# Optimization experiments

Measured on AMD Instinct MI355X. Metric: run time of the kernel, lower is better.

## Reference

```python
import jax, jax.numpy as jnp
import numpy as np

TAU = 2.0
VTH = 1.0
EPS = 1e-5
T_STEPS = 64

@jax.custom_vjp
def spike_atan(x):
    # Heaviside spike with ATan surrogate gradient (spikingjelly surrogate.ATan, alpha=2.0)
    return (x >= 0.0).astype(x.dtype)

def _spike_fwd(x):
    return spike_atan(x), x

def _spike_bwd(x, g):
    # d/dx [1/pi * atan(pi/2 * alpha * x) + 1/2] with alpha=2 -> 1 / (1 + (pi*x)^2)
    return (g / (1.0 + (jnp.pi * x) ** 2),)

spike_atan.defvjp(_spike_fwd, _spike_bwd)

def bn_eval(x, g, b, m, v):
    return (x - m) * (g / jnp.sqrt(v + EPS)) + b

def setup_inputs() -> dict:
    key = jax.random.key(0)
    ks = jax.random.split(key, 16)
    N, C, L, H, NC = 16384, 22, 63, 64, 4
    D = C * L
    s1 = 1.0 / np.sqrt(D)
    s2 = 1.0 / np.sqrt(H)
    return {
        'x': jax.random.normal(ks[0], (N, C, L), jnp.float32),
        'fc1_w': jax.random.normal(ks[1], (H, D), jnp.float32) * s1,
        'fc1_b': jax.random.normal(ks[2], (H,), jnp.float32) * s1,
        'bn1_g': jax.random.uniform(ks[3], (H,), jnp.float32, 0.5, 1.5),
        'bn1_b': jax.random.normal(ks[4], (H,), jnp.float32) * 0.1,
        'bn1_m': jax.random.normal(ks[5], (H,), jnp.float32) * 0.1,
        'bn1_v': jax.random.uniform(ks[6], (H,), jnp.float32, 0.5, 1.5),
        'fc2_w': jax.random.normal(ks[7], (H, H), jnp.float32) * s2,
        'fc2_b': jax.random.normal(ks[8], (H,), jnp.float32) * s2,
        'bn2_g': jax.random.uniform(ks[9], (H,), jnp.float32, 0.5, 1.5),
        'bn2_b': jax.random.normal(ks[10], (H,), jnp.float32) * 0.1,
        'bn2_m': jax.random.normal(ks[11], (H,), jnp.float32) * 0.1,
        'bn2_v': jax.random.uniform(ks[12], (H,), jnp.float32, 0.5, 1.5),
        'cls_w': jax.random.normal(ks[13], (NC, H), jnp.float32) * s2,
        'cls_b': jax.random.normal(ks[14], (NC,), jnp.float32) * s2,
    }

def reference(x, fc1_w, fc1_b, bn1_g, bn1_b, bn1_m, bn1_v,
              fc2_w, fc2_b, bn2_g, bn2_b, bn2_m, bn2_v, cls_w, cls_b):
    N = x.shape[0]
    x_flat = x.reshape(N, -1)                       # [N, 1386]
    # fc1+bn1 input is identical every timestep -> compute once
    a1 = bn_eval(x_flat @ fc1_w.T + fc1_b, bn1_g, bn1_b, bn1_m, bn1_v)  # [N, 64]

    def step(carry, _):
        v1, v2 = carry
        # LIF 1 (decay_input=True, hard reset to 0)
        h1 = v1 + (a1 - v1) / TAU
        s1 = spike_atan(h1 - VTH)
        v1n = h1 * (1.0 - s1)
        # fc2 + bn2 (eval mode; dropout inactive in inference)
        z = bn_eval(s1 @ fc2_w.T + fc2_b, bn2_g, bn2_b, bn2_m, bn2_v)
        # LIF 2
        h2 = v2 + (z - v2) / TAU
        s2 = spike_atan(h2 - VTH)
        v2n = h2 * (1.0 - s2)
        return (v1n, v2n), s2

    v0 = jnp.zeros_like(a1)
    _, out_seq = jax.lax.scan(step, (v0, v0), None, length=T_STEPS)  # [T, N, 64]
    logits = jnp.einsum('tnh,ch->tnc', out_seq, cls_w) + cls_b        # [T, N, 4]
    return logits.mean(axis=0)                                        # [N, 4]
```

## Files before the change

kernel.cpp:

```cpp
#include <hip/hip_runtime.h>
#include <hip/hip_bf16.h>

#define D_IN 1386
#define EPS 1e-5f
#define CHUNKS 44

typedef __attribute__((ext_vector_type(8))) short short8v;
typedef __attribute__((ext_vector_type(4))) float f32x4;
typedef unsigned short ushortt;

__device__ inline unsigned short bf16rne(float f) {
    unsigned int u = __float_as_uint(f);
    u += 0x7FFFu + ((u >> 16) & 1u);
    return (unsigned short)(u >> 16);
}
__device__ inline float bfbits_to_f(unsigned short b) {
    return __uint_as_float(((unsigned int)b) << 16);
}

union S8U { short8v s; unsigned int u[4]; };

__device__ inline unsigned int cvt2(float v0, float v1, float& r0, float& r1) {
    union { __hip_bfloat162 b2; unsigned int u; } cv;
    cv.b2 = __float22bfloat162_rn(make_float2(v0, v1));
    r0 = v0 - __uint_as_float((cv.u & 0xFFFFu) << 16);
    r1 = v1 - __uint_as_float(cv.u & 0xFFFF0000u);
    return cv.u;
}
__device__ inline unsigned int cvt2n(float v0, float v1) {
    union { __hip_bfloat162 b2; unsigned int u; } cv;
    cv.b2 = __float22bfloat162_rn(make_float2(v0, v1));
    return cv.u;
}

__global__ __launch_bounds__(256) void prep_w3(const float* __restrict__ w,
                                               ushortt* __restrict__ w3) {
    int idx = blockIdx.x * 256 + threadIdx.x;
    if (idx >= CHUNKS * 6144) return;
    int c   = idx / 6144;
    int rem = idx - c * 6144;
    int g   = rem >> 9;
    int l   = (rem >> 3) & 63;
    int j   = rem & 7;
    int T   = g / 3, s = g - 3 * T;
    int h   = 16 * T + (l & 15);
    int k   = 32 * c + 8 * (l >> 4) + j;
    float v = (k < D_IN) ? w[h * D_IN + k] : 0.f;
    unsigned short hh = bf16rne(v);
    float r1 = v - bfbits_to_f(hh);
    unsigned short mm = bf16rne(r1);
    float r2 = r1 - bfbits_to_f(mm);
    unsigned short ll = bf16rne(r2);
    w3[idx] = (s == 0) ? hh : (s == 1) ? mm : ll;
}

__global__ __launch_bounds__(512, 4) void fc1_mfma(const float* __restrict__ x,
                                                   const ushortt* __restrict__ w3,
                                                   float* __restrict__ y) {
    const int lane = threadIdx.x & 63;
    const int wid  = threadIdx.x >> 6;
    const int T    = wid & 3;
    const int sg   = wid >> 2;
    const int n0   = blockIdx.x * 32 + sg * 16;
    const int r    = lane & 15;
    const int g4   = lane >> 4;
    const float* xrow = x + (size_t)(n0 + r) * D_IN + 8 * g4;
    const ushortt* wT = w3 + 3 * T * 512;

    f32x4 acc = (f32x4){0.f, 0.f, 0.f, 0.f};

    float   a[6][8];
    short8v B[3][3];

    auto issueA = [&](int c, int s) {
        if (c < CHUNKS - 1) {
            const float2* p = (const float2*)(xrow + 32 * c);
            float2 v0 = p[0], v1 = p[1], v2 = p[2], v3 = p[3];
            a[s][0] = v0.x; a[s][1] = v0.y; a[s][2] = v1.x; a[s][3] = v1.y;
            a[s][4] = v2.x; a[s][5] = v2.y; a[s][6] = v3.x; a[s][7] = v3.y;
        } else {
            const float* p = xrow + 32 * (CHUNKS - 1);
#pragma unroll
            for (int j = 0; j < 8; ++j) {
                int kk = 8 * g4 + j;
                a[s][j] = (kk < D_IN - 32 * (CHUNKS - 1)) ? p[j] : 0.f;
            }
        }
    };
    auto issueB = [&](int c, int s) {
        const short8v* bp = (const short8v*)(wT + (size_t)c * 6144) + lane;
        B[s][0] = bp[0];
        B[s][1] = bp[64];
        B[s][2] = bp[128];
    };
    auto body = [&](int sa, int sb) {
        S8U Ah, Am, Al;
#pragma unroll
        for (int d = 0; d < 4; ++d) {
            float m0, m1, l0, l1;
            Ah.u[d] = cvt2(a[sa][2 * d], a[sa][2 * d + 1], m0, m1);
            Am.u[d] = cvt2(m0, m1, l0, l1);
            Al.u[d] = cvt2n(l0, l1);
        }
        const short8v XH = Ah.s, XM = Am.s, XL = Al.s;
        const short8v Bh = B[sb][0], Bm = B[sb][1], Bl = B[sb][2];
        acc = __builtin_amdgcn_mfma_f32_16x16x32_bf16(XL, Bh, acc, 0, 0, 0);
        acc = __builtin_amdgcn_mfma_f32_16x16x32_bf16(XM, Bm, acc, 0, 0, 0);
        acc = __builtin_amdgcn_mfma_f32_16x16x32_bf16(XH, Bl, acc, 0, 0, 0);
        acc = __builtin_amdgcn_mfma_f32_16x16x32_bf16(XM, Bh, acc, 0, 0, 0);
        acc = __builtin_amdgcn_mfma_f32_16x16x32_bf16(XH, Bm, acc, 0, 0, 0);
        acc = __builtin_amdgcn_mfma_f32_16x16x32_bf16(XH, Bh, acc, 0, 0, 0);
    };

#pragma unroll
    for (int c = 0; c < 6; ++c) issueA(c, c);
#pragma unroll
    for (int c = 0; c < 3; ++c) issueB(c, c);

#pragma unroll
    for (int c = 0; c < CHUNKS; ++c) {
        body(c % 6, c % 3);
        if (c + 6 < CHUNKS) issueA(c + 6, c % 6);
        if (c + 3 < CHUNKS) issueB(c + 3, c % 3);
    }

#pragma unroll
    for (int q = 0; q < 4; ++q)
        y[(size_t)(n0 + 4 * g4 + q) * 64 + 16 * T + r] = acc[q];
}

__global__ __launch_bounds__(256, 4) void snn_kernel(
    const float* __restrict__ y,
    const float* __restrict__ fc1_b,
    const float* __restrict__ bn1_g, const float* __restrict__ bn1_b,
    const float* __restrict__ bn1_m, const float* __restrict__ bn1_v,
    const float* __restrict__ fc2_w, const float* __restrict__ fc2_b,
    const float* __restrict__ bn2_g, const float* __restrict__ bn2_b,
    const float* __restrict__ bn2_m, const float* __restrict__ bn2_v,
    const float* __restrict__ cls_w, const float* __restrict__ cls_b,
    float* __restrict__ out)
{
    __shared__ unsigned int spk[2][16][36];
    __shared__ float redc[4][16][4];
    const int lane = threadIdx.x & 63;
    const int T    = threadIdx.x >> 6;
    const int n0   = blockIdx.x * 16;
    const int r    = lane & 15;
    const int grp  = lane >> 4;

    short8v Whi[2], Wlo[2];
    {
        const int hp = 16 * T + r;
        const float scale = bn2_g[hp] / sqrtf(bn2_v[hp] + EPS);
#pragma unroll
        for (int Hh = 0; Hh < 2; ++Hh) {
            S8U hi, lo;
#pragma unroll
            for (int d = 0; d < 4; ++d) {
                const int kk = 32 * Hh + 8 * grp + 2 * d;
                float w0 = fc2_w[hp * 64 + kk]     * scale;
                float w1 = fc2_w[hp * 64 + kk + 1] * scale;
                unsigned short h0 = bf16rne(w0), h1 = bf16rne(w1);
                unsigned short l0 = bf16rne(w0 - bfbits_to_f(h0));
                unsigned short l1 = bf16rne(w1 - bfbits_to_f(h1));
                hi.u[d] = (unsigned int)h0 | ((unsigned int)h1 << 16);
                lo.u[d] = (unsigned int)l0 | ((unsigned int)l1 << 16);
            }
            Whi[Hh] = hi.s;
            Wlo[Hh] = lo.s;
        }
    }

    const int h0 = 16 * T + 4 * grp;
    float a1[4], biasD[4];
    {
        float4 yv = *(const float4*)&y[(size_t)(n0 + r) * 64 + h0];
#pragma unroll
        for (int q = 0; q < 4; ++q) {
            const int h = h0 + q;
            float s1v = bn1_g[h] / sqrtf(bn1_v[h] + EPS);
            float yq  = (q == 0) ? yv.x : (q == 1) ? yv.y : (q == 2) ? yv.z : yv.w;
            a1[q] = (yq + fc1_b[h] - bn1_m[h]) * s1v + bn1_b[h];
            const float s2v = bn2_g[h] / sqrtf(bn2_v[h] + EPS);
            biasD[q] = (fc2_b[h] - bn2_m[h]) * s2v + bn2_b[h];
        }
    }

    float v1[4], v2[4], cnt[4];
#pragma unroll
    for (int q = 0; q < 4; ++q) { v1[q] = 0.f; v2[q] = 0.f; cnt[q] = 0.f; }

    for (int t = 0; t < 64; ++t) {
        const int b = t & 1;
        unsigned int dw0, dw1;
        {
            float h1a = v1[0] + (a1[0] - v1[0]) * 0.5f;
            float h1b = v1[1] + (a1[1] - v1[1]) * 0.5f;
            float h1c = v1[2] + (a1[2] - v1[2]) * 0.5f;
            float h1d = v1[3] + (a1[3] - v1[3]) * 0.5f;
            bool sa = h1a >= 1.f, sb = h1b >= 1.f, sc = h1c >= 1.f, sd = h1d >= 1.f;
            v1[0] = sa ? 0.f : h1a; v1[1] = sb ? 0.f : h1b;
            v1[2] = sc ? 0.f : h1c; v1[3] = sd ? 0.f : h1d;
            dw0 = (sa ? 0x3F80u : 0u) | (sb ? 0x3F800000u : 0u);
            dw1 = (sc ? 0x3F80u : 0u) | (sd ? 0x3F800000u : 0u);
        }
        *(uint2*)&spk[b][r][8 * T + 2 * grp] = make_uint2(dw0, dw1);
        __syncthreads();
        uint4 wv0 = *(const uint4*)&spk[b][r][4 * grp];
        uint4 wv1 = *(const uint4*)&spk[b][r][16 + 4 * grp];
        S8U s0u, s1u;
        s0u.u[0] = wv0.x; s0u.u[1] = wv0.y; s0u.u[2] = wv0.z; s0u.u[3] = wv0.w;
        s1u.u[0] = wv1.x; s1u.u[1] = wv1.y; s1u.u[2] = wv1.z; s1u.u[3] = wv1.w;
        const short8v S0 = s0u.s, S1 = s1u.s;

        f32x4 c1;
        c1[0] = biasD[0]; c1[1] = biasD[1]; c1[2] = biasD[2]; c1[3] = biasD[3];
        f32x4 c2 = (f32x4){0.f, 0.f, 0.f, 0.f};
        c1 = __builtin_amdgcn_mfma_f32_16x16x32_bf16(Whi[0], S0, c1, 0, 0, 0);
        c2 = __builtin_amdgcn_mfma_f32_16x16x32_bf16(Wlo[0], S0, c2, 0, 0, 0);
        c1 = __builtin_amdgcn_mfma_f32_16x16x32_bf16(Whi[1], S1, c1, 0, 0, 0);
        c2 = __builtin_amdgcn_mfma_f32_16x16x32_bf16(Wlo[1], S1, c2, 0, 0, 0);

#pragma unroll
        for (int q = 0; q < 4; ++q) {
            float z  = c1[q] + c2[q];
            float h2 = v2[q] + (z - v2[q]) * 0.5f;
            bool s = h2 >= 1.f;
            v2[q] = s ? 0.f : h2;
            cnt[q] += s ? 1.f : 0.f;
        }
    }

    float p[4];
#pragma unroll
    for (int c = 0; c < 4; ++c) {
        p[c] = cnt[0] * cls_w[c * 64 + h0]     + cnt[1] * cls_w[c * 64 + h0 + 1]
             + cnt[2] * cls_w[c * 64 + h0 + 2] + cnt[3] * cls_w[c * 64 + h0 + 3];
        p[c] += __shfl_xor(p[c], 16);
        p[c] += __shfl_xor(p[c], 32);
    }
    if (lane < 16) {
        float4 v; v.x = p[0]; v.y = p[1]; v.z = p[2]; v.w = p[3];
        *(float4*)&redc[T][lane][0] = v;
    }
    __syncthreads();
    if (threadIdx.x < 16) {
        const int s = threadIdx.x;
        float4 o;
        o.x = (redc[0][s][0] + redc[1][s][0] + redc[2][s][0] + redc[3][s][0]) * (1.f / 64.f) + cls_b[0];
        o.y = (redc[0][s][1] + redc[1][s][1] + redc[2][s][1] + redc[3][s][1]) * (1.f / 64.f) + cls_b[1];
        o.z = (redc[0][s][2] + redc[1][s][2] + redc[2][s][2] + redc[3][s][2]) * (1.f / 64.f) + cls_b[2];
        o.w = (redc[0][s][3] + redc[1][s][3] + redc[2][s][3] + redc[3][s][3]) * (1.f / 64.f) + cls_b[3];
        *(float4*)&out[(size_t)(n0 + s) * 4] = o;
    }
}

extern "C" void kernel_launch(void* const* d_in, const int* in_sizes, int n_in,
                              void* d_out, int out_size, void* d_ws, size_t ws_size,
                              hipStream_t stream) {
    const float* x     = (const float*)d_in[0];
    const float* fc1_w = (const float*)d_in[1];
    const float* fc1_b = (const float*)d_in[2];
    const float* bn1_g = (const float*)d_in[3];
    const float* bn1_b = (const float*)d_in[4];
    const float* bn1_m = (const float*)d_in[5];
    const float* bn1_v = (const float*)d_in[6];
    const float* fc2_w = (const float*)d_in[7];
    const float* fc2_b = (const float*)d_in[8];
    const float* bn2_g = (const float*)d_in[9];
    const float* bn2_b = (const float*)d_in[10];
    const float* bn2_m = (const float*)d_in[11];
    const float* bn2_v = (const float*)d_in[12];
    const float* cls_w = (const float*)d_in[13];
    const float* cls_b = (const float*)d_in[14];

    float*   y  = (float*)d_ws;
    ushortt* w3 = (ushortt*)((char*)d_ws + (4 << 20));

    prep_w3 <<<1056, 256, 0, stream>>>(fc1_w, w3);
    fc1_mfma<<<512,  512, 0, stream>>>(x, w3, y);
    snn_kernel<<<1024, 256, 0, stream>>>(y, fc1_b, bn1_g, bn1_b, bn1_m, bn1_v,
                                         fc2_w, fc2_b, bn2_g, bn2_b, bn2_m, bn2_v,
                                         cls_w, cls_b, (float*)d_out);
}
```

Baseline: 91.75 us.

## Share split-bf16 X tile via LDS across four output-column waves

Each 256-thread block now handles 16 rows. Threads cooperatively load x, split it into three bf16 parts and write them once into double-buffered shared memory, and the four waves (one per 16-column tile) read the shared A fragments. Before, each wave loaded and converted the same x rows itself, which duplicated global reads and conversion work fourfold. The cost is a __syncthreads every chunk, a shallower prefetch depth (two chunks instead of six), and a change in grid and block shape.

After: 75.32 us. 17.9% less time.

```diff
diff --git a/kernel.cpp b/kernel.cpp
--- a/kernel.cpp
+++ b/kernel.cpp
@@ -54,56 +54,57 @@
     w3[idx] = (s == 0) ? hh : (s == 1) ? mm : ll;
 }
 
-__global__ __launch_bounds__(512, 4) void fc1_mfma(const float* __restrict__ x,
+__global__ __launch_bounds__(256, 4) void fc1_mfma(const float* __restrict__ x,
                                                    const ushortt* __restrict__ w3,
                                                    float* __restrict__ y) {
-    const int lane = threadIdx.x & 63;
-    const int wid  = threadIdx.x >> 6;
-    const int T    = wid & 3;
-    const int sg   = wid >> 2;
-    const int n0   = blockIdx.x * 32 + sg * 16;
+    __shared__ ushortt asp[2][3][16][40];
+    const int t    = threadIdx.x;
+    const int lane = t & 63;
+    const int T    = t >> 6;
+    const int n0   = blockIdx.x * 16;
     const int r    = lane & 15;
     const int g4   = lane >> 4;
-    const float* xrow = x + (size_t)(n0 + r) * D_IN + 8 * g4;
-    const ushortt* wT = w3 + 3 * T * 512;
+    const int srow = t >> 4;
+    const int kp   = t & 15;
+    const float* xs = x + (size_t)(n0 + srow) * D_IN + 2 * kp;
 
     f32x4 acc = (f32x4){0.f, 0.f, 0.f, 0.f};
-
-    float   a[6][8];
-    short8v B[3][3];
-
-    auto issueA = [&](int c, int s) {
+    short8v Br[2][3];
+    float fA0, fA1, fB0, fB1;
+
+    auto stage_load = [&](int c, bool pa) {
+        float v0 = 0.f, v1 = 0.f;
         if (c < CHUNKS - 1) {
-            const float2* p = (const float2*)(xrow + 32 * c);
-            float2 v0 = p[0], v1 = p[1], v2 = p[2], v3 = p[3];
-            a[s][0] = v0.x; a[s][1] = v0.y; a[s][2] = v1.x; a[s][3] = v1.y;
-            a[s][4] = v2.x; a[s][5] = v2.y; a[s][6] = v3.x; a[s][7] = v3.y;
+            float2 v = *(const float2*)(xs + 32 * c);
+            v0 = v.x; v1 = v.y;
         } else {
-            const float* p = xrow + 32 * (CHUNKS - 1);
-#pragma unroll
-            for (int j = 0; j < 8; ++j) {
-                int kk = 8 * g4 + j;
-                a[s][j] = (kk < D_IN - 32 * (CHUNKS - 1)) ? p[j] : 0.f;
-            }
-        }
+            int k0 = 32 * c + 2 * kp;
+            if (k0 < D_IN)     v0 = xs[32 * c];
+            if (k0 + 1 < D_IN) v1 = xs[32 * c + 1];
+        }
+        if (pa) { fA0 = v0; fA1 = v1; } else { fB0 = v0; fB1 = v1; }
+    };
+    auto stage_write = [&](int nb, bool pa) {
+        float u0 = pa ? fA0 : fB0, u1 = pa ? fA1 : fB1;
+        float m0, m1, l0, l1;
+        unsigned int hi = cvt2(u0, u1, m0, m1);
+        unsigned int mi = cvt2(m0, m1, l0, l1);
+        unsigned int lo = cvt2n(l0, l1);
+        *(unsigned int*)&asp[nb][0][srow][2 * kp] = hi;
+        *(unsigned int*)&asp[nb][1][srow][2 * kp] = mi;
+        *(unsigned int*)&asp[nb][2][srow][2 * kp] = lo;
     };
     auto issueB = [&](int c, int s) {
-        const short8v* bp = (const short8v*)(wT + (size_t)c * 6144) + lane;
-        B[s][0] = bp[0];
-        B[s][1] = bp[64];
-        B[s][2] = bp[128];
-    };
-    auto body = [&](int sa, int sb) {
-        S8U Ah, Am, Al;
-#pragma unroll
-        for (int d = 0; d < 4; ++d) {
-            float m0, m1, l0, l1;
-            Ah.u[d] = cvt2(a[sa][2 * d], a[sa][2 * d + 1], m0, m1);
-            Am.u[d] = cvt2(m0, m1, l0, l1);
-            Al.u[d] = cvt2n(l0, l1);
-        }
-        const short8v XH = Ah.s, XM = Am.s, XL = Al.s;
-        const short8v Bh = B[sb][0], Bm = B[sb][1], Bl = B[sb][2];
+        const short8v* bp = (const short8v*)(w3 + (size_t)c * 6144 + 3 * T * 512) + lane;
+        Br[s][0] = bp[0];
+        Br[s][1] = bp[64];
+        Br[s][2] = bp[128];
+    };
+    auto compute = [&](int cb, int sb) {
+        const short8v XH = *(const short8v*)&asp[cb][0][r][8 * g4];
+        const short8v XM = *(const short8v*)&asp[cb][1][r][8 * g4];
+        const short8v XL = *(const short8v*)&asp[cb][2][r][8 * g4];
+        const short8v Bh = Br[sb][0], Bm = Br[sb][1], Bl = Br[sb][2];
         acc = __builtin_amdgcn_mfma_f32_16x16x32_bf16(XL, Bh, acc, 0, 0, 0);
         acc = __builtin_amdgcn_mfma_f32_16x16x32_bf16(XM, Bm, acc, 0, 0, 0);
         acc = __builtin_amdgcn_mfma_f32_16x16x32_bf16(XH, Bl, acc, 0, 0, 0);
@@ -112,16 +113,22 @@
         acc = __builtin_amdgcn_mfma_f32_16x16x32_bf16(XH, Bh, acc, 0, 0, 0);
     };
 
-#pragma unroll
-    for (int c = 0; c < 6; ++c) issueA(c, c);
-#pragma unroll
-    for (int c = 0; c < 3; ++c) issueB(c, c);
+    stage_load(0, true);
+    stage_write(0, true);
+    stage_load(1, false);
+    issueB(0, 0);
+    issueB(1, 1);
+    __syncthreads();
 
 #pragma unroll
     for (int c = 0; c < CHUNKS; ++c) {
-        body(c % 6, c % 3);
-        if (c + 6 < CHUNKS) issueA(c + 6, c % 6);
-        if (c + 3 < CHUNKS) issueB(c + 3, c % 3);
+        const int cb = c & 1;
+        const bool pa = (cb == 0);
+        compute(cb, cb);
+        if (c + 2 < CHUNKS) stage_load(c + 2, pa);
+        if (c + 2 < CHUNKS) issueB(c + 2, cb);
+        if (c + 1 < CHUNKS) stage_write(cb ^ 1, !pa);
+        __syncthreads();
     }
 
 #pragma unroll
@@ -278,7 +285,7 @@
     ushortt* w3 = (ushortt*)((char*)d_ws + (4 << 20));
 
     prep_w3 <<<1056, 256, 0, stream>>>(fc1_w, w3);
-    fc1_mfma<<<512,  512, 0, stream>>>(x, w3, y);
+    fc1_mfma<<<1024, 256, 0, stream>>>(x, w3, y);
     snn_kernel<<<1024, 256, 0, stream>>>(y, fc1_b, bn1_g, bn1_b, bn1_m, bn1_v,
                                          fc2_w, fc2_b, bn2_g, bn2_b, bn2_m, bn2_v,
                                          cls_w, cls_b, (float*)d_out);
```
